# Optimization experiments

Measured on AMD Instinct MI355X. Metric: run time of the kernel, lower is better.

Reference implementation:

```python
import jax, jax.numpy as jnp
import numpy as np
import math

N_EXP = 64
TOP_K = 2
EVAL_CAPACITY = 1.25
MIN_CAPACITY = 4


def _capacity(num_tokens):
    cap = math.floor(TOP_K * EVAL_CAPACITY * num_tokens / N_EXP)
    cap += cap % 2
    return max(cap, MIN_CAPACITY)


def setup_inputs() -> dict:
    key = jax.random.key(0)
    k1, k2 = jax.random.split(key)
    x = jax.random.normal(k1, (4096, 2048), dtype=jnp.float32)
    w_g = jax.random.normal(k2, (64, 2048), dtype=jnp.float32) * 0.02
    return {"x": x, "w_g": w_g}


def reference(x, w_g):
    # x: [T, D], w_g: [E, D]
    T, D = x.shape
    cap = _capacity(T)

    logits = x @ w_g.T                                   # [T, E]
    top_v, top_i = jax.lax.top_k(logits, TOP_K)          # [T, K]

    # softmax over only the top-k logits (others -> -inf)
    rows = jnp.arange(T)[:, None]
    masked = jnp.full_like(logits, -jnp.inf).at[rows, top_i].set(top_v)
    router_probs = jax.nn.softmax(masked, axis=-1)       # [T, E]

    # Capacity-aware assignment: flatten (token, k) pairs in row-major order,
    # exactly matching the original sequential double loop. The slot for each
    # attempt is the exclusive prefix count of attempts to that expert; once an
    # expert's count exceeds capacity, all later attempts are rejected, which
    # matches the sequential semantics (usage only stops growing at capacity).
    flat_e = top_i.reshape(-1)                           # [T*K]
    tok = jnp.repeat(jnp.arange(T), TOP_K)               # [T*K]
    onehot = jax.nn.one_hot(flat_e, N_EXP, dtype=jnp.int32)   # [T*K, E]
    cum = jnp.cumsum(onehot, axis=0)                     # inclusive counts
    slot = cum[jnp.arange(T * TOP_K), flat_e] - 1        # exclusive prefix count
    assigned = slot < cap

    used_capacity = jnp.minimum(cum[-1], cap).astype(jnp.int32)   # [E]

    # Route rejected attempts to a scratch slot `cap`, then slice it off.
    safe_slot = jnp.where(assigned, slot, cap)
    w = router_probs[tok, flat_e]                        # [T*K]

    cb_weight = (jnp.zeros((T, N_EXP, cap + 1), dtype=x.dtype)
                 .at[tok, flat_e, safe_slot].set(w))[..., :cap]
    sec_mask = (jnp.zeros((T, N_EXP, cap + 1), dtype=bool)
                .at[tok, flat_e, safe_slot].set(True))[..., :cap]

    return used_capacity, cb_weight, sec_mask
```

## Files before the change

### kernel.cpp

```cpp
#include <hip/hip_runtime.h>
#include <math.h>

#define T_TOK 4096
#define D_DIM 2048
#define NEXP  64
#define CAP   160

#define NG 128
#define NZ 2048
#define BM 32
#define BN 64
#define BK 32

__global__ __launch_bounds__(256) void fused_main(
    const float* __restrict__ x, const float* __restrict__ wg,
    float* __restrict__ out, int out_size,
    int* __restrict__ topi, float* __restrict__ topw)
{
    const int bid = blockIdx.x;
    const int tid = threadIdx.x;

    if (bid >= NG) {
        const int zb = bid - NG;
        const size_t n4 = (size_t)out_size >> 2;
        float4* o4 = (float4*)out;
        const float4 z = make_float4(0.f, 0.f, 0.f, 0.f);
        const size_t stride = (size_t)NZ * 256;
        for (size_t i = (size_t)zb * 256 + tid; i < n4; i += stride)
            o4[i] = z;
        if (zb == 0 && tid == 0) {
            for (size_t i = n4 << 2; i < (size_t)out_size; ++i) out[i] = 0.f;
        }
        return;
    }

    __shared__ float sA[BK][BM + 1];
    __shared__ float sB[BK][BN + 1];
    __shared__ float sL[BM][BN + 1];

    const int t0 = bid * BM;
    const int tx = tid & 15;
    const int ty = tid >> 4;

    float acc[2][4];
#pragma unroll
    for (int r = 0; r < 2; ++r)
#pragma unroll
        for (int j = 0; j < 4; ++j) acc[r][j] = 0.f;

    for (int k0 = 0; k0 < D_DIM; k0 += BK) {
        {
            const int m  = tid >> 3;
            const int kk = (tid & 7) << 2;
            const float4 v = *(const float4*)(x + (size_t)(t0 + m) * D_DIM + k0 + kk);
            sA[kk + 0][m] = v.x; sA[kk + 1][m] = v.y;
            sA[kk + 2][m] = v.z; sA[kk + 3][m] = v.w;
        }
#pragma unroll
        for (int r = 0; r < 2; ++r) {
            const int e  = (tid >> 3) + r * 32;
            const int kk = (tid & 7) << 2;
            const float4 v = *(const float4*)(wg + (size_t)e * D_DIM + k0 + kk);
            sB[kk + 0][e] = v.x; sB[kk + 1][e] = v.y;
            sB[kk + 2][e] = v.z; sB[kk + 3][e] = v.w;
        }
        __syncthreads();
#pragma unroll
        for (int kk = 0; kk < BK; ++kk) {
            const float a0 = sA[kk][2 * ty];
            const float a1 = sA[kk][2 * ty + 1];
            const float b0 = sB[kk][4 * tx + 0];
            const float b1 = sB[kk][4 * tx + 1];
            const float b2 = sB[kk][4 * tx + 2];
            const float b3 = sB[kk][4 * tx + 3];
            acc[0][0] += a0 * b0; acc[0][1] += a0 * b1;
            acc[0][2] += a0 * b2; acc[0][3] += a0 * b3;
            acc[1][0] += a1 * b0; acc[1][1] += a1 * b1;
            acc[1][2] += a1 * b2; acc[1][3] += a1 * b3;
        }
        __syncthreads();
    }

#pragma unroll
    for (int r = 0; r < 2; ++r)
#pragma unroll
        for (int j = 0; j < 4; ++j)
            sL[2 * ty + r][4 * tx + j] = acc[r][j];
    __syncthreads();

    if (tid < BM) {
        const int m = tid;
        float v1 = -INFINITY, v2 = -INFINITY;
        int i1 = 0, i2 = 0;
        for (int e = 0; e < NEXP; ++e) {
            const float v = sL[m][e];
            if (v > v1)      { v2 = v1; i2 = i1; v1 = v; i1 = e; }
            else if (v > v2) { v2 = v;  i2 = e; }
        }
        const float r  = expf(v2 - v1);
        const float s  = 1.0f / (1.0f + r);
        const int   gt = t0 + m;
        topi[2 * gt + 0] = i1;
        topi[2 * gt + 1] = i2;
        topw[2 * gt + 0] = s;
        topw[2 * gt + 1] = r * s;
    }
}

__global__ __launch_bounds__(64) void scatter_assign(
    const int* __restrict__ topi, const float* __restrict__ topw,
    float* __restrict__ out)
{
    __shared__ int cnt[NEXP];
    const int lane = threadIdx.x;
    cnt[lane] = 0;
    __syncthreads();

    float* __restrict__ cb   = out + NEXP;
    float* __restrict__ mask = out + NEXP + (size_t)T_TOK * NEXP * CAP;

    const unsigned long long lt = ((unsigned long long)1 << lane) - 1ull;

    for (int c = 0; c < (T_TOK * 2) / 64; ++c) {
        const int f = c * 64 + lane;
        const int e = topi[f];

        unsigned long long m = ~0ull;
#pragma unroll
        for (int b = 0; b < 6; ++b) {
            const unsigned long long vb = __ballot((e >> b) & 1);
            m &= ((e >> b) & 1) ? vb : ~vb;
        }
        const int p     = __popcll(m & lt);
        const int total = __popcll(m);
        const int base  = cnt[e];
        const int slot  = base + p;
        if (p == 0) cnt[e] = base + total;

        if (slot < CAP) {
            const int t = f >> 1;
            const size_t off = ((size_t)t * NEXP + e) * CAP + slot;
            cb[off]   = topw[f];
            mask[off] = 1.0f;
        }
        __syncthreads();
    }

    int used = cnt[lane];
    if (used > CAP) used = CAP;
    out[lane] = (float)used;
}

extern "C" void kernel_launch(void* const* d_in, const int* in_sizes, int n_in,
                              void* d_out, int out_size, void* d_ws, size_t ws_size,
                              hipStream_t stream)
{
    const float* x  = (const float*)d_in[0];
    const float* wg = (const float*)d_in[1];
    float* out = (float*)d_out;

    int*   topi = (int*)d_ws;
    float* topw = (float*)(topi + T_TOK * 2);

    fused_main<<<NG + NZ, 256, 0, stream>>>(x, wg, out, out_size, topi, topw);
    scatter_assign<<<1, 64, 0, stream>>>(topi, topw, out);
}
```

Before: 536.8 us.

## Restructure gating GEMM per-lane experts with wave-reduce top-2 and nontemporal zeroing

Replaces the shared-memory tiled GEMM with a scheme where each block handles 4 tokens and each lane owns one expert. Each wave covers a quarter of D, and the partial sums are reduced through shared memory. Top-2 selection becomes a wave shuffle reduction instead of a serial loop in 32 threads. The output zeroing uses nontemporal stores, and the scatter kernel prefetches the next chunk and drops a redundant barrier. The per-lane x reads are uniform scalar loads and weights are re-read from L2 for every block, which risks lower arithmetic reuse than the tiled GEMM.

```diff
diff --git a/kernel.cpp b/kernel.cpp
--- a/kernel.cpp
+++ b/kernel.cpp
@@ -6,11 +6,11 @@
 #define NEXP  64
 #define CAP   160
 
-#define NG 128
-#define NZ 2048
-#define BM 32
-#define BN 64
-#define BK 32
+#define TPB   4
+#define NGB   (T_TOK / TPB)
+#define NZB   2048
+
+typedef float vfloat4 __attribute__((ext_vector_type(4)));
 
 __global__ __launch_bounds__(256) void fused_main(
     const float* __restrict__ x, const float* __restrict__ wg,
@@ -20,90 +20,85 @@
     const int bid = blockIdx.x;
     const int tid = threadIdx.x;
 
-    if (bid >= NG) {
-        const int zb = bid - NG;
+    if (bid >= NGB) {
+        const int zb = bid - NGB;
         const size_t n4 = (size_t)out_size >> 2;
-        float4* o4 = (float4*)out;
-        const float4 z = make_float4(0.f, 0.f, 0.f, 0.f);
-        const size_t stride = (size_t)NZ * 256;
+        vfloat4* o4 = (vfloat4*)out;
+        const vfloat4 z = {0.f, 0.f, 0.f, 0.f};
+        const size_t stride = (size_t)NZB * 256;
         for (size_t i = (size_t)zb * 256 + tid; i < n4; i += stride)
-            o4[i] = z;
+            __builtin_nontemporal_store(z, &o4[i]);
         if (zb == 0 && tid == 0) {
             for (size_t i = n4 << 2; i < (size_t)out_size; ++i) out[i] = 0.f;
         }
         return;
     }
 
-    __shared__ float sA[BK][BM + 1];
-    __shared__ float sB[BK][BN + 1];
-    __shared__ float sL[BM][BN + 1];
+    const int e    = tid & 63;
+    const int w    = __builtin_amdgcn_readfirstlane(tid >> 6);
+    const int tok0 = bid * TPB;
+    const int wk0  = w * (D_DIM / 4);
 
-    const int t0 = bid * BM;
-    const int tx = tid & 15;
-    const int ty = tid >> 4;
+    float acc[TPB] = {0.f, 0.f, 0.f, 0.f};
 
-    float acc[2][4];
+    const float* __restrict__ wrow = wg + (size_t)e * D_DIM + wk0;
+
+    for (int c = 0; c < (D_DIM / 4) / 32; ++c) {
+        vfloat4 b[8];
 #pragma unroll
-    for (int r = 0; r < 2; ++r)
+        for (int j = 0; j < 8; ++j)
+            b[j] = *(const vfloat4*)(wrow + c * 32 + j * 4);
 #pragma unroll
-        for (int j = 0; j < 4; ++j) acc[r][j] = 0.f;
-
-    for (int k0 = 0; k0 < D_DIM; k0 += BK) {
-        {
-            const int m  = tid >> 3;
-            const int kk = (tid & 7) << 2;
-            const float4 v = *(const float4*)(x + (size_t)(t0 + m) * D_DIM + k0 + kk);
-            sA[kk + 0][m] = v.x; sA[kk + 1][m] = v.y;
-            sA[kk + 2][m] = v.z; sA[kk + 3][m] = v.w;
+        for (int t = 0; t < TPB; ++t) {
+            const float* __restrict__ xp =
+                x + (size_t)(tok0 + t) * D_DIM + wk0 + c * 32;
+            float s = 0.f;
+#pragma unroll
+            for (int j = 0; j < 8; ++j) {
+                s += xp[j*4+0] * b[j].x + xp[j*4+1] * b[j].y
+                   + xp[j*4+2] * b[j].z + xp[j*4+3] * b[j].w;
+            }
+            acc[t] += s;
         }
-#pragma unroll
-        for (int r = 0; r < 2; ++r) {
-            const int e  = (tid >> 3) + r * 32;
-            const int kk = (tid & 7) << 2;
-            const float4 v = *(const float4*)(wg + (size_t)e * D_DIM + k0 + kk);
-            sB[kk + 0][e] = v.x; sB[kk + 1][e] = v.y;
-            sB[kk + 2][e] = v.z; sB[kk + 3][e] = v.w;
-        }
-        __syncthreads();
-#pragma unroll
-        for (int kk = 0; kk < BK; ++kk) {
-            const float a0 = sA[kk][2 * ty];
-            const float a1 = sA[kk][2 * ty + 1];
-            const float b0 = sB[kk][4 * tx + 0];
-            const float b1 = sB[kk][4 * tx + 1];
-            const float b2 = sB[kk][4 * tx + 2];
-            const float b3 = sB[kk][4 * tx + 3];
-            acc[0][0] += a0 * b0; acc[0][1] += a0 * b1;
-            acc[0][2] += a0 * b2; acc[0][3] += a0 * b3;
-            acc[1][0] += a1 * b0; acc[1][1] += a1 * b1;
-            acc[1][2] += a1 * b2; acc[1][3] += a1 * b3;
-        }
-        __syncthreads();
     }
 
+    __shared__ float sAcc[4][TPB][NEXP];
 #pragma unroll
-    for (int r = 0; r < 2; ++r)
-#pragma unroll
-        for (int j = 0; j < 4; ++j)
-            sL[2 * ty + r][4 * tx + j] = acc[r][j];
+    for (int t = 0; t < TPB; ++t)
+        sAcc[w][t][e] = acc[t];
     __syncthreads();
 
-    if (tid < BM) {
-        const int m = tid;
-        float v1 = -INFINITY, v2 = -INFINITY;
-        int i1 = 0, i2 = 0;
-        for (int e = 0; e < NEXP; ++e) {
-            const float v = sL[m][e];
-            if (v > v1)      { v2 = v1; i2 = i1; v1 = v; i1 = e; }
-            else if (v > v2) { v2 = v;  i2 = e; }
-        }
+    const int t = w;
+    float v = sAcc[0][t][e] + sAcc[1][t][e] + sAcc[2][t][e] + sAcc[3][t][e];
+
+    float v1 = v;         int i1 = e;
+    float v2 = -INFINITY; int i2 = NEXP;
+#pragma unroll
+    for (int off = 32; off >= 1; off >>= 1) {
+        const float ov1 = __shfl_xor(v1, off, 64);
+        const int   oi1 = __shfl_xor(i1, off, 64);
+        const float ov2 = __shfl_xor(v2, off, 64);
+        const int   oi2 = __shfl_xor(i2, off, 64);
+        const bool firstMine = (v1 > ov1) || (v1 == ov1 && i1 < oi1);
+        const float n1  = firstMine ? v1  : ov1;
+        const int   ni1 = firstMine ? i1  : oi1;
+        const float c1  = firstMine ? ov1 : v1;
+        const int   ci1 = firstMine ? oi1 : i1;
+        const float c2  = firstMine ? v2  : ov2;
+        const int   ci2 = firstMine ? i2  : oi2;
+        const bool secondC1 = (c1 > c2) || (c1 == c2 && ci1 < ci2);
+        v1 = n1;                      i1 = ni1;
+        v2 = secondC1 ? c1 : c2;      i2 = secondC1 ? ci1 : ci2;
+    }
+
+    if (e == 0) {
+        const int gt = tok0 + t;
         const float r  = expf(v2 - v1);
-        const float s  = 1.0f / (1.0f + r);
-        const int   gt = t0 + m;
+        const float s1 = 1.0f / (1.0f + r);
         topi[2 * gt + 0] = i1;
         topi[2 * gt + 1] = i2;
-        topw[2 * gt + 0] = s;
-        topw[2 * gt + 1] = r * s;
+        topw[2 * gt + 0] = s1;
+        topw[2 * gt + 1] = r * s1;
     }
 }
 
@@ -120,10 +115,18 @@
     float* __restrict__ mask = out + NEXP + (size_t)T_TOK * NEXP * CAP;
 
     const unsigned long long lt = ((unsigned long long)1 << lane) - 1ull;
+    const int NCH = (T_TOK * 2) / 64;
 
-    for (int c = 0; c < (T_TOK * 2) / 64; ++c) {
-        const int f = c * 64 + lane;
-        const int e = topi[f];
+    int   e  = topi[lane];
+    float tw = topw[lane];
+
+    for (int c = 0; c < NCH; ++c) {
+        int   en  = 0;
+        float twn = 0.f;
+        if (c + 1 < NCH) {
+            en  = topi[(c + 1) * 64 + lane];
+            twn = topw[(c + 1) * 64 + lane];
+        }
 
         unsigned long long m = ~0ull;
 #pragma unroll
@@ -132,18 +135,18 @@
             m &= ((e >> b) & 1) ? vb : ~vb;
         }
         const int p     = __popcll(m & lt);
-        const int total = __popcll(m);
         const int base  = cnt[e];
         const int slot  = base + p;
-        if (p == 0) cnt[e] = base + total;
+        if (p == 0) cnt[e] = base + __popcll(m);
 
         if (slot < CAP) {
+            const int f = c * 64 + lane;
             const int t = f >> 1;
             const size_t off = ((size_t)t * NEXP + e) * CAP + slot;
-            cb[off]   = topw[f];
+            cb[off]   = tw;
             mask[off] = 1.0f;
         }
-        __syncthreads();
+        e = en; tw = twn;
     }
 
     int used = cnt[lane];
@@ -162,6 +165,6 @@
     int*   topi = (int*)d_ws;
     float* topw = (float*)(topi + T_TOK * 2);
 
-    fused_main<<<NG + NZ, 256, 0, stream>>>(x, wg, out, out_size, topi, topw);
+    fused_main<<<NGB + NZB, 256, 0, stream>>>(x, wg, out, out_size, topi, topw);
     scatter_assign<<<1, 64, 0, stream>>>(topi, topw, out);
 }
```

Result: faster. 459.9 us (-14.3%).
